# Kernel tuning notes

Hardware: AMD Instinct MI355X
Metric: run time of the kernel (lower is better)

Reference implementation:

```python
import jax, jax.numpy as jnp
import numpy as np

D_MODEL, D_FF, NUM_EXPERTS, RANK, TOP_K = 1024, 4096, 8, 16, 2
B, S = 8, 2048


def _expert_ffn(h, wi_w, wo_w, A, Bm):
    # h: [B,S,D]; wi_w: [F,D]; wo_w: [D,F]; A: [R,D]; Bm: [F,R]
    inter = jnp.einsum('bsd,fd->bsf', h, wi_w)
    lora = jnp.einsum('bsr,fr->bsf', jnp.einsum('bsd,rd->bsr', h, A), Bm)
    inter = jax.nn.relu(inter + lora)
    return jnp.einsum('bsf,df->bsd', inter, wo_w)


def setup_inputs() -> dict:
    key = jax.random.key(0)
    ks = jax.random.split(key, 8)
    hidden_states = jax.random.normal(ks[0], (B, S, D_MODEL), dtype=jnp.float32)
    wi_w = jax.random.normal(ks[1], (D_FF, D_MODEL), dtype=jnp.float32) * (1.0 / np.sqrt(D_MODEL))
    wo_w = jax.random.normal(ks[2], (D_MODEL, D_FF), dtype=jnp.float32) * (1.0 / np.sqrt(D_FF))
    # kaiming-uniform-ish A; B random (zeros in init, randomized for a meaningful kernel baseline)
    lora_As = jax.random.uniform(ks[3], (NUM_EXPERTS, RANK, D_MODEL), dtype=jnp.float32, minval=-1.0, maxval=1.0) / np.sqrt(D_MODEL)
    lora_Bs = jax.random.normal(ks[4], (NUM_EXPERTS, D_FF, RANK), dtype=jnp.float32) * 0.02
    top_k_indices = jnp.arange(TOP_K, dtype=jnp.int32)  # task-level selected experts, shape [top_k]
    top_k_values = jax.random.uniform(ks[5], (TOP_K,), dtype=jnp.float32)
    return {'hidden_states': hidden_states, 'wi_w': wi_w, 'wo_w': wo_w,
            'lora_As': lora_As, 'lora_Bs': lora_Bs,
            'top_k_indices': top_k_indices, 'top_k_values': top_k_values}


def reference(hidden_states, wi_w, wo_w, lora_As, lora_Bs, top_k_indices, top_k_values):
    # Task-level top-k: each selected expert runs a full LoRA-augmented FFN over
    # all tokens, scaled by its scalar mixed routing weight, then summed.
    # sum_k v_k * ffn_{idx_k}(h) == sum_i (sum_{k: idx_k=i} v_k) * ffn_i(h)  (matches torch loop)
    out = jnp.zeros_like(hidden_states)
    for k in range(top_k_values.shape[0]):
        A = jnp.take(lora_As, top_k_indices[k], axis=0)
        Bm = jnp.take(lora_Bs, top_k_indices[k], axis=0)
        out = out + top_k_values[k] * _expert_ffn(hidden_states, wi_w, wo_w, A, Bm)
    return out
```

## Files before the change

### kernel.cpp

```cpp
#include <hip/hip_runtime.h>
#include <hip/hip_bf16.h>
#include <cstdint>
#include <cstddef>

#define D_MODEL 1024
#define D_FF    4096
#define RANK    16
#define NTOK    16384

typedef __attribute__((ext_vector_type(8))) __bf16 bf16x8;
typedef __attribute__((ext_vector_type(4))) float  f32x4;

using gas_t = const __attribute__((address_space(1))) void*;
using las_t = __attribute__((address_space(3))) void*;

__device__ __forceinline__ unsigned short f2bf(float f) {
    unsigned int u = __builtin_bit_cast(unsigned int, f);
    u += 0x7fffu + ((u >> 16) & 1u);
    return (unsigned short)(u >> 16);
}

__device__ __forceinline__ void gload_lds16(const unsigned short* g, unsigned short* l) {
    __builtin_amdgcn_global_load_lds((gas_t)g, (las_t)l, 16, 0, 0);
}

__global__ void cast_kernel(const float* __restrict__ in, unsigned short* __restrict__ out, int n4) {
    int i = blockIdx.x * blockDim.x + threadIdx.x;
    int stride = gridDim.x * blockDim.x;
    for (; i < n4; i += stride) {
        float4 v = reinterpret_cast<const float4*>(in)[i];
        ushort4 o;
        o.x = f2bf(v.x); o.y = f2bf(v.y); o.z = f2bf(v.z); o.w = f2bf(v.w);
        reinterpret_cast<ushort4*>(out)[i] = o;
    }
}

__global__ void lora_t_kernel(const float* __restrict__ h, const float* __restrict__ As,
                              const int* __restrict__ idx, unsigned short* __restrict__ tcat,
                              unsigned short* __restrict__ hbf) {
    const int m = blockIdx.x;
    const int l = threadIdx.x;
    float hreg[16];
    #pragma unroll
    for (int j = 0; j < 16; ++j) hreg[j] = h[(size_t)m * D_MODEL + j * 64 + l];
    #pragma unroll
    for (int j = 0; j < 16; ++j) hbf[(size_t)m * D_MODEL + j * 64 + l] = f2bf(hreg[j]);
    #pragma unroll
    for (int e = 0; e < 2; ++e) {
        const float* A = As + (size_t)idx[e] * RANK * D_MODEL;
        for (int r = 0; r < RANK; ++r) {
            float s = 0.f;
            #pragma unroll
            for (int j = 0; j < 16; ++j) s += hreg[j] * A[r * D_MODEL + j * 64 + l];
            #pragma unroll
            for (int off = 32; off >= 1; off >>= 1) s += __shfl_xor(s, off, 64);
            if (l == 0) tcat[(size_t)m * 32 + e * 16 + r] = f2bf(s);
        }
    }
}

__global__ void bcat_kernel(const float* __restrict__ Bs, const int* __restrict__ idx,
                            unsigned short* __restrict__ bcat) {
    int i = blockIdx.x * blockDim.x + threadIdx.x;
    if (i >= D_FF * 32) return;
    int f = i >> 5, kk = i & 31;
    int e = kk >> 4, r = kk & 15;
    bcat[i] = f2bf(Bs[(size_t)idx[e] * D_FF * RANK + (size_t)f * RANK + r]);
}

template<int KDIM, int EPI, int OSTRIDE, int GN>
__launch_bounds__(512, 2)
__global__ void gemm256(const unsigned short* __restrict__ A,
                        const unsigned short* __restrict__ Bm,
                        float* __restrict__ outF,
                        unsigned short* __restrict__ outBf,
                        const unsigned short* __restrict__ tcat,
                        const unsigned short* __restrict__ bcat,
                        const float* __restrict__ topv) {
    __shared__ unsigned short lds[2][2][2][128 * 64];
    const int tid  = threadIdx.x;
    const int lane = tid & 63;
    const int wid  = tid >> 6;
    const int wr   = wid >> 2;
    const int wc   = wid & 3;
    const int lr   = lane & 15;
    const int hi   = lane >> 4;
    const int swz  = (lane & 7) << 3;

    const int nwg  = gridDim.x;
    const int orig = blockIdx.x;
    const int wg   = (orig & 7) * (nwg >> 3) + (orig >> 3);
    const int bm0  = (wg / GN) * 256;
    const int bn0  = (wg % GN) * 256;

    constexpr int NKT = KDIM / 64;
    constexpr int NT2 = NKT / 2;

    f32x4 acc[8][4] = {};
    bf16x8 aF[8], b0[4], b1[4];

    auto stage = [&](int buf, int mat, int half, const unsigned short* src, int kt) {
        const int row0 = (mat == 0 ? bm0 : bn0) + half * 128;
        const int k0 = kt * 64;
        #pragma unroll
        for (int p = 0; p < 2; ++p) {
            const int L = p * 8192 + tid * 16;
            const int r = L >> 7;
            const int c = (L & 127) >> 1;
            const int gc = k0 + (c ^ ((r & 7) << 3));
            gload_lds16(src + (size_t)(row0 + r) * KDIM + gc,
                        &lds[buf][mat][half][0] + (L >> 1));
        }
    };
    auto readA = [&](int buf, int qm) {
        #pragma unroll
        for (int fr = 0; fr < 4; ++fr)
            #pragma unroll
            for (int ks = 0; ks < 2; ++ks)
                aF[fr * 2 + ks] = *reinterpret_cast<const bf16x8*>(
                    &lds[buf][0][wr][(qm * 64 + fr * 16 + lr) * 64 + ((ks * 32 + hi * 8) ^ swz)]);
    };
    auto readB = [&](int buf, int qn, bf16x8* bb) {
        #pragma unroll
        for (int fc = 0; fc < 2; ++fc)
            #pragma unroll
            for (int ks = 0; ks < 2; ++ks)
                bb[fc * 2 + ks] = *reinterpret_cast<const bf16x8*>(
                    &lds[buf][1][wc >> 1][((wc & 1) * 64 + qn * 32 + fc * 16 + lr) * 64
                                          + ((ks * 32 + hi * 8) ^ swz)]);
    };
    auto mfma16 = [&](int qm, int qn, const bf16x8* bb) {
        #pragma unroll
        for (int fr = 0; fr < 4; ++fr)
            #pragma unroll
            for (int fc = 0; fc < 2; ++fc)
                #pragma unroll
                for (int ks = 0; ks < 2; ++ks)
                    acc[qm * 4 + fr][qn * 2 + fc] = __builtin_amdgcn_mfma_f32_16x16x32_bf16(
                        aF[fr * 2 + ks], bb[fc * 2 + ks], acc[qm * 4 + fr][qn * 2 + fc], 0, 0, 0);
    };

#define BAR() __builtin_amdgcn_s_barrier()
#define WAIT_LGKM() do { asm volatile("s_waitcnt lgkmcnt(0)" ::: "memory"); \
                         __builtin_amdgcn_sched_barrier(0); } while (0)
#define WAIT_VM(n) do { asm volatile("s_waitcnt vmcnt(" #n ")" ::: "memory"); \
                        __builtin_amdgcn_sched_barrier(0); } while (0)
#define PRIO_MFMA(qm, qn, bb) do { __builtin_amdgcn_s_setprio(1); mfma16(qm, qn, bb); \
                                   __builtin_amdgcn_s_setprio(0); } while (0)

    stage(0, 0, 0, A, 0);  stage(0, 0, 1, A, 0);
    stage(0, 1, 0, Bm, 0); stage(0, 1, 1, Bm, 0);
    stage(1, 1, 0, Bm, 1); stage(1, 1, 1, Bm, 1);
    WAIT_VM(4);
    BAR();

    #pragma unroll 1
    for (int it = 0; it < NT2; ++it) {
        const int t1 = 2 * it + 1;
        const int t2 = (2 * it + 2 < NKT) ? 2 * it + 2 : NKT - 1;
        const int t3 = (2 * it + 3 < NKT) ? 2 * it + 3 : NKT - 1;
        readA(0, 0); readB(0, 0, b0);
        stage(1, 0, 0, A, t1);
        BAR(); WAIT_LGKM(); PRIO_MFMA(0, 0, b0); BAR();
        readB(0, 1, b1);
        stage(1, 0, 1, A, t1);
        BAR(); WAIT_LGKM(); PRIO_MFMA(0, 1, b1); BAR();
        readA(0, 1);
        stage(0, 1, 0, Bm, t2);
        BAR(); WAIT_LGKM(); PRIO_MFMA(1, 0, b0); BAR();
        stage(0, 1, 1, Bm, t2);
        BAR(); PRIO_MFMA(1, 1, b1); WAIT_VM(4); BAR();
        readA(1, 0); readB(1, 0, b0);
        stage(0, 0, 0, A, t2);
        BAR(); WAIT_LGKM(); PRIO_MFMA(0, 0, b0); BAR();
        readB(1, 1, b1);
        stage(0, 0, 1, A, t2);
        BAR(); WAIT_LGKM(); PRIO_MFMA(0, 1, b1); BAR();
        readA(1, 1);
        stage(1, 1, 0, Bm, t3);
        BAR(); WAIT_LGKM(); PRIO_MFMA(1, 0, b0); BAR();
        stage(1, 1, 1, Bm, t3);
        BAR(); PRIO_MFMA(1, 1, b1); WAIT_VM(4); BAR();
    }
    asm volatile("s_waitcnt vmcnt(0)" ::: "memory");
    __builtin_amdgcn_sched_barrier(0);
    BAR();

    const int rbase = bm0 + wr * 128 + hi * 4;
    const int cbase = bn0 + wc * 64 + lr;

    if constexpr (EPI == 1) {
        const float v0 = topv[0], v1 = topv[1];
        const bf16x8 z8 = {};
        bf16x8 bl0[4], bl1[4];
        #pragma unroll
        for (int ni = 0; ni < 4; ++ni) {
            const int f = cbase + ni * 16;
            bf16x8 bfull = *reinterpret_cast<const bf16x8*>(&bcat[(size_t)f * 32 + hi * 8]);
            bl0[ni] = (hi < 2) ? bfull : z8;
            bl1[ni] = (hi < 2) ? z8 : bfull;
        }
        #pragma unroll
        for (int mi = 0; mi < 8; ++mi) {
            const int mrow = bm0 + wr * 128 + mi * 16 + lr;
            const bf16x8 alo = *reinterpret_cast<const bf16x8*>(&tcat[(size_t)mrow * 32 + hi * 8]);
            #pragma unroll
            for (int ni = 0; ni < 4; ++ni) {
                const f32x4 zz = {};
                f32x4 l0 = __builtin_amdgcn_mfma_f32_16x16x32_bf16(alo, bl0[ni], zz, 0, 0, 0);
                f32x4 l1 = __builtin_amdgcn_mfma_f32_16x16x32_bf16(alo, bl1[ni], zz, 0, 0, 0);
                #pragma unroll
                for (int j = 0; j < 4; ++j) {
                    float z = acc[mi][ni][j];
                    float c = v0 * fmaxf(z + l0[j], 0.f) + v1 * fmaxf(z + l1[j], 0.f);
                    outBf[(size_t)(rbase + mi * 16 + j) * OSTRIDE + cbase + ni * 16] = f2bf(c);
                }
            }
        }
    } else {
        #pragma unroll
        for (int mi = 0; mi < 8; ++mi)
            #pragma unroll
            for (int ni = 0; ni < 4; ++ni)
                #pragma unroll
                for (int j = 0; j < 4; ++j)
                    outF[(size_t)(rbase + mi * 16 + j) * OSTRIDE + cbase + ni * 16] = acc[mi][ni][j];
    }
#undef BAR
#undef WAIT_LGKM
#undef WAIT_VM
#undef PRIO_MFMA
}

extern "C" void kernel_launch(void* const* d_in, const int* in_sizes, int n_in,
                              void* d_out, int out_size, void* d_ws, size_t ws_size,
                              hipStream_t stream) {
    const float* h    = (const float*)d_in[0];
    const float* wi   = (const float*)d_in[1];
    const float* wo   = (const float*)d_in[2];
    const float* As   = (const float*)d_in[3];
    const float* Bs   = (const float*)d_in[4];
    const int*   idx  = (const int*)d_in[5];
    const float* topv = (const float*)d_in[6];
    float* out = (float*)d_out;

    char* ws = (char*)d_ws;
    unsigned short* hbf  = (unsigned short*)(ws);
    unsigned short* wibf = (unsigned short*)(ws + 33554432);
    unsigned short* wobf = (unsigned short*)(ws + 41943040);
    unsigned short* tcat = (unsigned short*)(ws + 50331648);
    unsigned short* bcat = (unsigned short*)(ws + 51380224);
    unsigned short* comb = (unsigned short*)(ws + 51642368);

    lora_t_kernel<<<NTOK, 64, 0, stream>>>(h, As, idx, tcat, hbf);
    cast_kernel<<<1024, 256, 0, stream>>>(wi, wibf, (D_FF * D_MODEL) / 4);
    cast_kernel<<<1024, 256, 0, stream>>>(wo, wobf, (D_MODEL * D_FF) / 4);
    bcat_kernel<<<(D_FF * 32) / 256, 256, 0, stream>>>(Bs, idx, bcat);

    gemm256<D_MODEL, 1, D_FF, 16><<<dim3(64 * 16), 512, 0, stream>>>(
        hbf, wibf, nullptr, comb, tcat, bcat, topv);
    gemm256<D_FF, 0, D_MODEL, 4><<<dim3(64 * 4), 512, 0, stream>>>(
        comb, wobf, out, nullptr, nullptr, nullptr, nullptr);
}
```

Measured before the change: 348.2 us.

## Switch GEMMs to 32x32 MFMA, persist first GEMM over N tiles, MFMA LoRA-down

```diff
diff --git a/kernel.cpp b/kernel.cpp
--- a/kernel.cpp
+++ b/kernel.cpp
@@ -8,8 +8,9 @@
 #define RANK    16
 #define NTOK    16384
 
-typedef __attribute__((ext_vector_type(8))) __bf16 bf16x8;
-typedef __attribute__((ext_vector_type(4))) float  f32x4;
+typedef __attribute__((ext_vector_type(8)))  __bf16 bf16x8;
+typedef __attribute__((ext_vector_type(4)))  float  f32x4;
+typedef __attribute__((ext_vector_type(16))) float  f32x16;
 
 using gas_t = const __attribute__((address_space(1))) void*;
 using las_t = __attribute__((address_space(3))) void*;
@@ -35,40 +36,51 @@
     }
 }
 
-__global__ void lora_t_kernel(const float* __restrict__ h, const float* __restrict__ As,
-                              const int* __restrict__ idx, unsigned short* __restrict__ tcat,
-                              unsigned short* __restrict__ hbf) {
-    const int m = blockIdx.x;
-    const int l = threadIdx.x;
-    float hreg[16];
+__global__ void prep_kernel(const float* __restrict__ Bs, const float* __restrict__ As,
+                            const int* __restrict__ idx,
+                            unsigned short* __restrict__ bcat, unsigned short* __restrict__ acatg) {
+    int i = blockIdx.x * blockDim.x + threadIdx.x;
+    if (i < D_FF * 32) {
+        int f = i >> 5, kk = i & 31, e = kk >> 4, r = kk & 15;
+        bcat[i] = f2bf(Bs[(size_t)idx[e] * D_FF * RANK + (size_t)f * RANK + r]);
+    } else {
+        int j = i - D_FF * 32;
+        int row = j >> 10, col = j & 1023, e = row >> 4, r = row & 15;
+        acatg[j] = f2bf(As[(size_t)idx[e] * RANK * D_MODEL + r * D_MODEL + col]);
+    }
+}
+
+__global__ void lora_t_v2(const float* __restrict__ h,
+                          const unsigned short* __restrict__ acatg,
+                          unsigned short* __restrict__ tcat,
+                          unsigned short* __restrict__ hbf) {
+    const int tid = threadIdx.x, lane = tid & 63, w = tid >> 6;
+    const int tok0 = blockIdx.x * 64 + w * 16;
+    const int lr = lane & 15, kc = lane >> 4;
+    f32x4 acc0 = {}, acc1 = {};
+    const size_t rowoff = (size_t)(tok0 + lr) * D_MODEL;
+    #pragma unroll 4
+    for (int kt = 0; kt < 32; ++kt) {
+        const int k0 = kt * 32 + kc * 8;
+        float4 u0 = *reinterpret_cast<const float4*>(h + rowoff + k0);
+        float4 u1 = *reinterpret_cast<const float4*>(h + rowoff + k0 + 4);
+        union { bf16x8 v; unsigned short s[8]; } af;
+        af.s[0] = f2bf(u0.x); af.s[1] = f2bf(u0.y); af.s[2] = f2bf(u0.z); af.s[3] = f2bf(u0.w);
+        af.s[4] = f2bf(u1.x); af.s[5] = f2bf(u1.y); af.s[6] = f2bf(u1.z); af.s[7] = f2bf(u1.w);
+        *reinterpret_cast<bf16x8*>(&hbf[rowoff + k0]) = af.v;
+        bf16x8 b0 = *reinterpret_cast<const bf16x8*>(&acatg[(size_t)lr * D_MODEL + k0]);
+        bf16x8 b1 = *reinterpret_cast<const bf16x8*>(&acatg[(size_t)(16 + lr) * D_MODEL + k0]);
+        acc0 = __builtin_amdgcn_mfma_f32_16x16x32_bf16(af.v, b0, acc0, 0, 0, 0);
+        acc1 = __builtin_amdgcn_mfma_f32_16x16x32_bf16(af.v, b1, acc1, 0, 0, 0);
+    }
     #pragma unroll
-    for (int j = 0; j < 16; ++j) hreg[j] = h[(size_t)m * D_MODEL + j * 64 + l];
-    #pragma unroll
-    for (int j = 0; j < 16; ++j) hbf[(size_t)m * D_MODEL + j * 64 + l] = f2bf(hreg[j]);
-    #pragma unroll
-    for (int e = 0; e < 2; ++e) {
-        const float* A = As + (size_t)idx[e] * RANK * D_MODEL;
-        for (int r = 0; r < RANK; ++r) {
-            float s = 0.f;
-            #pragma unroll
-            for (int j = 0; j < 16; ++j) s += hreg[j] * A[r * D_MODEL + j * 64 + l];
-            #pragma unroll
-            for (int off = 32; off >= 1; off >>= 1) s += __shfl_xor(s, off, 64);
-            if (l == 0) tcat[(size_t)m * 32 + e * 16 + r] = f2bf(s);
-        }
-    }
-}
-
-__global__ void bcat_kernel(const float* __restrict__ Bs, const int* __restrict__ idx,
-                            unsigned short* __restrict__ bcat) {
-    int i = blockIdx.x * blockDim.x + threadIdx.x;
-    if (i >= D_FF * 32) return;
-    int f = i >> 5, kk = i & 31;
-    int e = kk >> 4, r = kk & 15;
-    bcat[i] = f2bf(Bs[(size_t)idx[e] * D_FF * RANK + (size_t)f * RANK + r]);
-}
-
-template<int KDIM, int EPI, int OSTRIDE, int GN>
+    for (int j = 0; j < 4; ++j) {
+        tcat[(size_t)(tok0 + kc * 4 + j) * 32 + lr]      = f2bf(acc0[j]);
+        tcat[(size_t)(tok0 + kc * 4 + j) * 32 + 16 + lr] = f2bf(acc1[j]);
+    }
+}
+
+template<int KDIM, int EPI, int GN_BASE, int NTILE, int OSTRIDE>
 __launch_bounds__(512, 2)
 __global__ void gemm256(const unsigned short* __restrict__ A,
                         const unsigned short* __restrict__ Bm,
@@ -83,25 +95,24 @@
     const int wid  = tid >> 6;
     const int wr   = wid >> 2;
     const int wc   = wid & 3;
-    const int lr   = lane & 15;
-    const int hi   = lane >> 4;
+    const int l31  = lane & 31;
+    const int hi2  = lane >> 5;
     const int swz  = (lane & 7) << 3;
 
     const int nwg  = gridDim.x;
     const int orig = blockIdx.x;
     const int wg   = (orig & 7) * (nwg >> 3) + (orig >> 3);
-    const int bm0  = (wg / GN) * 256;
-    const int bn0  = (wg % GN) * 256;
+    const int bm0  = (wg / GN_BASE) * 256;
+    const int wgn  = wg % GN_BASE;
 
     constexpr int NKT = KDIM / 64;
     constexpr int NT2 = NKT / 2;
 
-    f32x4 acc[8][4] = {};
+    const f32x16 zz16 = {};
+    f32x16 acc[4][2] = {};
     bf16x8 aF[8], b0[4], b1[4];
 
-    auto stage = [&](int buf, int mat, int half, const unsigned short* src, int kt) {
-        const int row0 = (mat == 0 ? bm0 : bn0) + half * 128;
-        const int k0 = kt * 64;
+    auto stage = [&](int buf, int mat, int half, const unsigned short* src, int row0, int k0) {
         #pragma unroll
         for (int p = 0; p < 2; ++p) {
             const int L = p * 8192 + tid * 16;
@@ -114,30 +125,26 @@
     };
     auto readA = [&](int buf, int qm) {
         #pragma unroll
-        for (int fr = 0; fr < 4; ++fr)
-            #pragma unroll
-            for (int ks = 0; ks < 2; ++ks)
-                aF[fr * 2 + ks] = *reinterpret_cast<const bf16x8*>(
-                    &lds[buf][0][wr][(qm * 64 + fr * 16 + lr) * 64 + ((ks * 32 + hi * 8) ^ swz)]);
+        for (int d = 0; d < 2; ++d)
+            #pragma unroll
+            for (int ks = 0; ks < 4; ++ks)
+                aF[d * 4 + ks] = *reinterpret_cast<const bf16x8*>(
+                    &lds[buf][0][wr][(qm * 64 + d * 32 + l31) * 64 + ((ks * 16 + hi2 * 8) ^ swz)]);
     };
     auto readB = [&](int buf, int qn, bf16x8* bb) {
         #pragma unroll
-        for (int fc = 0; fc < 2; ++fc)
-            #pragma unroll
-            for (int ks = 0; ks < 2; ++ks)
-                bb[fc * 2 + ks] = *reinterpret_cast<const bf16x8*>(
-                    &lds[buf][1][wc >> 1][((wc & 1) * 64 + qn * 32 + fc * 16 + lr) * 64
-                                          + ((ks * 32 + hi * 8) ^ swz)]);
-    };
-    auto mfma16 = [&](int qm, int qn, const bf16x8* bb) {
-        #pragma unroll
-        for (int fr = 0; fr < 4; ++fr)
-            #pragma unroll
-            for (int fc = 0; fc < 2; ++fc)
-                #pragma unroll
-                for (int ks = 0; ks < 2; ++ks)
-                    acc[qm * 4 + fr][qn * 2 + fc] = __builtin_amdgcn_mfma_f32_16x16x32_bf16(
-                        aF[fr * 2 + ks], bb[fc * 2 + ks], acc[qm * 4 + fr][qn * 2 + fc], 0, 0, 0);
+        for (int ks = 0; ks < 4; ++ks)
+            bb[ks] = *reinterpret_cast<const bf16x8*>(
+                &lds[buf][1][wc >> 1][((wc & 1) * 64 + qn * 32 + l31) * 64
+                                      + ((ks * 16 + hi2 * 8) ^ swz)]);
+    };
+    auto mfma8 = [&](int qm, int qn, const bf16x8* bb) {
+        #pragma unroll
+        for (int ks = 0; ks < 4; ++ks)
+            #pragma unroll
+            for (int d = 0; d < 2; ++d)
+                acc[qm * 2 + d][qn] = __builtin_amdgcn_mfma_f32_32x32x16_bf16(
+                    aF[d * 4 + ks], bb[ks], acc[qm * 2 + d][qn], 0, 0, 0);
     };
 
 #define BAR() __builtin_amdgcn_s_barrier()
@@ -145,87 +152,105 @@
                          __builtin_amdgcn_sched_barrier(0); } while (0)
 #define WAIT_VM(n) do { asm volatile("s_waitcnt vmcnt(" #n ")" ::: "memory"); \
                         __builtin_amdgcn_sched_barrier(0); } while (0)
-#define PRIO_MFMA(qm, qn, bb) do { __builtin_amdgcn_s_setprio(1); mfma16(qm, qn, bb); \
+#define PRIO_MFMA(qm, qn, bb) do { __builtin_amdgcn_s_setprio(1); mfma8(qm, qn, bb); \
                                    __builtin_amdgcn_s_setprio(0); } while (0)
 
-    stage(0, 0, 0, A, 0);  stage(0, 0, 1, A, 0);
-    stage(0, 1, 0, Bm, 0); stage(0, 1, 1, Bm, 0);
-    stage(1, 1, 0, Bm, 1); stage(1, 1, 1, Bm, 1);
+    const int bn00 = wgn * 256;
+    stage(0, 0, 0, A, bm0, 0);         stage(0, 0, 1, A, bm0 + 128, 0);
+    stage(0, 1, 0, Bm, bn00, 0);       stage(0, 1, 1, Bm, bn00 + 128, 0);
+    stage(1, 1, 0, Bm, bn00, 64);      stage(1, 1, 1, Bm, bn00 + 128, 64);
     WAIT_VM(4);
     BAR();
 
+    float v0 = 0.f, v1 = 0.f;
+    if constexpr (EPI == 1) { v0 = topv[0]; v1 = topv[1]; }
+    const int mrow0 = bm0 + wr * 128;
+
     #pragma unroll 1
-    for (int it = 0; it < NT2; ++it) {
-        const int t1 = 2 * it + 1;
-        const int t2 = (2 * it + 2 < NKT) ? 2 * it + 2 : NKT - 1;
-        const int t3 = (2 * it + 3 < NKT) ? 2 * it + 3 : NKT - 1;
-        readA(0, 0); readB(0, 0, b0);
-        stage(1, 0, 0, A, t1);
-        BAR(); WAIT_LGKM(); PRIO_MFMA(0, 0, b0); BAR();
-        readB(0, 1, b1);
-        stage(1, 0, 1, A, t1);
-        BAR(); WAIT_LGKM(); PRIO_MFMA(0, 1, b1); BAR();
-        readA(0, 1);
-        stage(0, 1, 0, Bm, t2);
-        BAR(); WAIT_LGKM(); PRIO_MFMA(1, 0, b0); BAR();
-        stage(0, 1, 1, Bm, t2);
-        BAR(); PRIO_MFMA(1, 1, b1); WAIT_VM(4); BAR();
-        readA(1, 0); readB(1, 0, b0);
-        stage(0, 0, 0, A, t2);
-        BAR(); WAIT_LGKM(); PRIO_MFMA(0, 0, b0); BAR();
-        readB(1, 1, b1);
-        stage(0, 0, 1, A, t2);
-        BAR(); WAIT_LGKM(); PRIO_MFMA(0, 1, b1); BAR();
-        readA(1, 1);
-        stage(1, 1, 0, Bm, t3);
-        BAR(); WAIT_LGKM(); PRIO_MFMA(1, 0, b0); BAR();
-        stage(1, 1, 1, Bm, t3);
-        BAR(); PRIO_MFMA(1, 1, b1); WAIT_VM(4); BAR();
+    for (int tl = 0; tl < NTILE; ++tl) {
+        const int bn0 = (wgn + GN_BASE * tl) * 256;
+        const int bn_next = (tl + 1 < NTILE) ? bn0 + GN_BASE * 256 : bn0;
+
+        #pragma unroll 1
+        for (int it = 0; it < NT2; ++it) {
+            const bool last = (it == NT2 - 1);
+            const int t1k = (2 * it + 1) * 64;
+            const int tAk = last ? 0  : (2 * it + 2) * 64;
+            const int tBk = last ? 64 : (2 * it + 3) * 64;
+            const int bnS = last ? bn_next : bn0;
+            readA(0, 0); readB(0, 0, b0);
+            stage(1, 0, 0, A, bm0, t1k);
+            BAR(); WAIT_LGKM(); PRIO_MFMA(0, 0, b0); BAR();
+            readB(0, 1, b1);
+            stage(1, 0, 1, A, bm0 + 128, t1k);
+            BAR(); WAIT_LGKM(); PRIO_MFMA(0, 1, b1); BAR();
+            readA(0, 1);
+            stage(0, 1, 0, Bm, bnS, tAk);
+            BAR(); WAIT_LGKM(); PRIO_MFMA(1, 0, b0); BAR();
+            stage(0, 1, 1, Bm, bnS + 128, tAk);
+            BAR(); PRIO_MFMA(1, 1, b1); WAIT_VM(4); BAR();
+            readA(1, 0); readB(1, 0, b0);
+            stage(0, 0, 0, A, bm0, tAk);
+            BAR(); WAIT_LGKM(); PRIO_MFMA(0, 0, b0); BAR();
+            readB(1, 1, b1);
+            stage(0, 0, 1, A, bm0 + 128, tAk);
+            BAR(); WAIT_LGKM(); PRIO_MFMA(0, 1, b1); BAR();
+            readA(1, 1);
+            stage(1, 1, 0, Bm, bnS, tBk);
+            BAR(); WAIT_LGKM(); PRIO_MFMA(1, 0, b0); BAR();
+            stage(1, 1, 1, Bm, bnS + 128, tBk);
+            BAR(); PRIO_MFMA(1, 1, b1); WAIT_VM(4); BAR();
+        }
+
+        const int ncol0 = bn0 + wc * 64;
+        if constexpr (EPI == 1) {
+            bf16x8 tA0[4], tA1[4], bB0[2], bB1[2];
+            #pragma unroll
+            for (int mi = 0; mi < 4; ++mi) {
+                const size_t o = (size_t)(mrow0 + mi * 32 + l31) * 32 + hi2 * 8;
+                tA0[mi] = *reinterpret_cast<const bf16x8*>(&tcat[o]);
+                tA1[mi] = *reinterpret_cast<const bf16x8*>(&tcat[o + 16]);
+            }
+            #pragma unroll
+            for (int ni = 0; ni < 2; ++ni) {
+                const size_t o = (size_t)(ncol0 + ni * 32 + l31) * 32 + hi2 * 8;
+                bB0[ni] = *reinterpret_cast<const bf16x8*>(&bcat[o]);
+                bB1[ni] = *reinterpret_cast<const bf16x8*>(&bcat[o + 16]);
+            }
+            #pragma unroll
+            for (int mi = 0; mi < 4; ++mi)
+                #pragma unroll
+                for (int ni = 0; ni < 2; ++ni) {
+                    f32x16 l0 = __builtin_amdgcn_mfma_f32_32x32x16_bf16(tA0[mi], bB0[ni], zz16, 0, 0, 0);
+                    f32x16 l1 = __builtin_amdgcn_mfma_f32_32x32x16_bf16(tA1[mi], bB1[ni], zz16, 0, 0, 0);
+                    #pragma unroll
+                    for (int r = 0; r < 16; ++r) {
+                        const int grow = mrow0 + mi * 32 + (r & 3) + 8 * (r >> 2) + 4 * hi2;
+                        const int gcol = ncol0 + ni * 32 + l31;
+                        float z = acc[mi][ni][r];
+                        float c = v0 * fmaxf(z + l0[r], 0.f) + v1 * fmaxf(z + l1[r], 0.f);
+                        outBf[(size_t)grow * OSTRIDE + gcol] = f2bf(c);
+                    }
+                }
+        } else {
+            #pragma unroll
+            for (int mi = 0; mi < 4; ++mi)
+                #pragma unroll
+                for (int ni = 0; ni < 2; ++ni)
+                    #pragma unroll
+                    for (int r = 0; r < 16; ++r) {
+                        const int grow = mrow0 + mi * 32 + (r & 3) + 8 * (r >> 2) + 4 * hi2;
+                        const int gcol = ncol0 + ni * 32 + l31;
+                        outF[(size_t)grow * OSTRIDE + gcol] = acc[mi][ni][r];
+                    }
+        }
+        #pragma unroll
+        for (int mi = 0; mi < 4; ++mi)
+            #pragma unroll
+            for (int ni = 0; ni < 2; ++ni)
+                acc[mi][ni] = zz16;
     }
     asm volatile("s_waitcnt vmcnt(0)" ::: "memory");
-    __builtin_amdgcn_sched_barrier(0);
-    BAR();
-
-    const int rbase = bm0 + wr * 128 + hi * 4;
-    const int cbase = bn0 + wc * 64 + lr;
-
-    if constexpr (EPI == 1) {
-        const float v0 = topv[0], v1 = topv[1];
-        const bf16x8 z8 = {};
-        bf16x8 bl0[4], bl1[4];
-        #pragma unroll
-        for (int ni = 0; ni < 4; ++ni) {
-            const int f = cbase + ni * 16;
-            bf16x8 bfull = *reinterpret_cast<const bf16x8*>(&bcat[(size_t)f * 32 + hi * 8]);
-            bl0[ni] = (hi < 2) ? bfull : z8;
-            bl1[ni] = (hi < 2) ? z8 : bfull;
-        }
-        #pragma unroll
-        for (int mi = 0; mi < 8; ++mi) {
-            const int mrow = bm0 + wr * 128 + mi * 16 + lr;
-            const bf16x8 alo = *reinterpret_cast<const bf16x8*>(&tcat[(size_t)mrow * 32 + hi * 8]);
-            #pragma unroll
-            for (int ni = 0; ni < 4; ++ni) {
-                const f32x4 zz = {};
-                f32x4 l0 = __builtin_amdgcn_mfma_f32_16x16x32_bf16(alo, bl0[ni], zz, 0, 0, 0);
-                f32x4 l1 = __builtin_amdgcn_mfma_f32_16x16x32_bf16(alo, bl1[ni], zz, 0, 0, 0);
-                #pragma unroll
-                for (int j = 0; j < 4; ++j) {
-                    float z = acc[mi][ni][j];
-                    float c = v0 * fmaxf(z + l0[j], 0.f) + v1 * fmaxf(z + l1[j], 0.f);
-                    outBf[(size_t)(rbase + mi * 16 + j) * OSTRIDE + cbase + ni * 16] = f2bf(c);
-                }
-            }
-        }
-    } else {
-        #pragma unroll
-        for (int mi = 0; mi < 8; ++mi)
-            #pragma unroll
-            for (int ni = 0; ni < 4; ++ni)
-                #pragma unroll
-                for (int j = 0; j < 4; ++j)
-                    outF[(size_t)(rbase + mi * 16 + j) * OSTRIDE + cbase + ni * 16] = acc[mi][ni][j];
-    }
 #undef BAR
 #undef WAIT_LGKM
 #undef WAIT_VM
@@ -245,20 +270,21 @@
     float* out = (float*)d_out;
 
     char* ws = (char*)d_ws;
-    unsigned short* hbf  = (unsigned short*)(ws);
-    unsigned short* wibf = (unsigned short*)(ws + 33554432);
-    unsigned short* wobf = (unsigned short*)(ws + 41943040);
-    unsigned short* tcat = (unsigned short*)(ws + 50331648);
-    unsigned short* bcat = (unsigned short*)(ws + 51380224);
-    unsigned short* comb = (unsigned short*)(ws + 51642368);
-
-    lora_t_kernel<<<NTOK, 64, 0, stream>>>(h, As, idx, tcat, hbf);
+    unsigned short* hbf   = (unsigned short*)(ws);
+    unsigned short* wibf  = (unsigned short*)(ws + 33554432);
+    unsigned short* wobf  = (unsigned short*)(ws + 41943040);
+    unsigned short* tcat  = (unsigned short*)(ws + 50331648);
+    unsigned short* bcat  = (unsigned short*)(ws + 51380224);
+    unsigned short* acatg = (unsigned short*)(ws + 51642368);
+    unsigned short* comb  = (unsigned short*)(ws + 51707904);
+
+    prep_kernel<<<640, 256, 0, stream>>>(Bs, As, idx, bcat, acatg);
+    lora_t_v2<<<NTOK / 64, 256, 0, stream>>>(h, acatg, tcat, hbf);
     cast_kernel<<<1024, 256, 0, stream>>>(wi, wibf, (D_FF * D_MODEL) / 4);
     cast_kernel<<<1024, 256, 0, stream>>>(wo, wobf, (D_MODEL * D_FF) / 4);
-    bcat_kernel<<<(D_FF * 32) / 256, 256, 0, stream>>>(Bs, idx, bcat);
-
-    gemm256<D_MODEL, 1, D_FF, 16><<<dim3(64 * 16), 512, 0, stream>>>(
+
+    gemm256<D_MODEL, 1, 4, 4, D_FF><<<dim3(256), 512, 0, stream>>>(
         hbf, wibf, nullptr, comb, tcat, bcat, topv);
-    gemm256<D_FF, 0, D_MODEL, 4><<<dim3(64 * 4), 512, 0, stream>>>(
+    gemm256<D_FF, 0, 4, 1, D_MODEL><<<dim3(256), 512, 0, stream>>>(
         comb, wobf, out, nullptr, nullptr, nullptr, nullptr);
 }
```

Result: slower. 424.0 us (+21.8%).
